# Kernel optimization log

Hardware: AMD Instinct MI355X
Metric: run time of the kernel (lower is better)

Reference implementation:

```python
import jax, jax.numpy as jnp
import numpy as np

B, BOARD, D = 2048, 19, 64
N = BOARD * BOARD
DIRS = ((-1, 0), (1, 0), (0, -1), (0, 1))


def _shift(x, dr, dc, fill):
    # shift a [B,H,W] grid by (dr,dc), filling off-board with `fill`
    p = jnp.pad(x, ((0, 0), (1, 1), (1, 1)), constant_values=fill)
    H, W = x.shape[1], x.shape[2]
    return p[:, 1 + dr:1 + dr + H, 1 + dc:1 + dc + W]


def _group_labels(color):
    # batched parallel connected components (min-label propagation + pointer jumping)
    # color: [B,H,W] int32, -1 = empty, 0 = black, 1 = white
    b, H, W = color.shape
    n = H * W
    init = jnp.broadcast_to(jnp.arange(n, dtype=jnp.int32).reshape(1, H, W), (b, H, W))

    def body(state):
        labels, _ = state
        m = labels
        for dr, dc in DIRS:
            nl = _shift(labels, dr, dc, n)          # neighbor label (n = sentinel)
            nc = _shift(color, dr, dc, -2)          # neighbor color (-2 = off-board)
            m = jnp.minimum(m, jnp.where(nc == color, nl, n))
        flat = m.reshape(b, n)
        # pointer jumping: label <- label[label]
        flat = jnp.minimum(flat, jnp.take_along_axis(flat, flat, axis=1))
        new = flat.reshape(b, H, W)
        return new, jnp.any(new != labels)

    labels, _ = jax.lax.while_loop(lambda s: s[1], body, (init, jnp.array(True)))
    return labels.reshape(b, n)


def setup_inputs() -> dict:
    key = jax.random.key(0)
    k1, k2, k3, k4 = jax.random.split(key, 4)
    col = jax.random.randint(k1, (B, BOARD, BOARD), 0, 3)  # 0 empty, 1 black, 2 white
    stones = jnp.stack([col == 1, col == 2], axis=1)        # [B,2,H,W] bool
    ko_points = jax.random.randint(k2, (B, 2), -1, BOARD).astype(jnp.int32)
    current_player = jax.random.randint(k3, (B,), 0, 2).astype(jnp.int32)
    features = jax.random.normal(k4, (B, N, D), dtype=jnp.float32)
    return {"stones": stones, "ko_points": ko_points,
            "current_player": current_player, "features": features}


def reference(stones, ko_points, current_player, features):
    stones = stones.astype(bool)
    black = stones[:, 0]
    white = stones[:, 1] & ~stones[:, 0]
    color = jnp.where(black, 0, jnp.where(white, 1, -1)).astype(jnp.int32)  # [B,H,W]
    b, H, W = color.shape
    n = H * W
    bidx = jnp.arange(b)

    labels = _group_labels(color)                 # [B,N] flat root index per point
    empty = color < 0
    stone = ~empty
    lab_grid = labels.reshape(b, H, W)

    # liberties per group root: each empty point contributes 1 per DISTINCT adjacent group
    neigh = []
    for dr, dc in DIRS:
        nl = _shift(lab_grid, dr, dc, n)
        ns = _shift(stone.astype(jnp.int32), dr, dc, 0) > 0
        neigh.append(jnp.where(empty & ns, nl, n).reshape(b, n))
    libs = jnp.zeros((b, n), dtype=jnp.int32)
    for i in range(4):
        li = neigh[i]
        dup = jnp.zeros(li.shape, dtype=bool)
        for j in range(i):
            dup = dup | (li == neigh[j])
        contrib = ((li < n) & ~dup).astype(jnp.int32)
        libs = libs.at[bidx[:, None], jnp.where(li < n, li, 0)].add(contrib)

    # legal moves = empty points minus ko point
    legal = empty.reshape(b, n)
    kr, kc = ko_points[:, 0].astype(jnp.int32), ko_points[:, 1].astype(jnp.int32)
    has_ko = kr >= 0
    ko_flat = jnp.clip(kr, 0, H - 1) * W + jnp.clip(kc, 0, W - 1)
    cur = legal[bidx, ko_flat]
    legal = legal.at[bidx, ko_flat].set(jnp.where(has_ko, False, cur))

    scores = jnp.stack([black.sum(axis=(1, 2)), white.sum(axis=(1, 2))], axis=1).astype(jnp.int32)

    # group sum-pooling of per-point features over union-find groups
    mask = stone.reshape(b, n).astype(features.dtype)[..., None]   # [B,N,1]
    pooled = jnp.zeros_like(features).at[bidx[:, None], labels].add(features * mask)
    out_feats = jnp.take_along_axis(pooled, labels[..., None], axis=1) * mask

    return out_feats, libs, legal, scores
```

## Files before the change

kernel.cpp:

```cpp
#include <hip/hip_runtime.h>


constexpr int BOARD = 19;
constexpr int NN = BOARD * BOARD;
constexpr int DD = 64;
constexpr int NT = 256;
constexpr int NW = NT / 64;
constexpr int NQ = NN * (DD / 4);

typedef float f4v __attribute__((ext_vector_type(4)));

__global__ __launch_bounds__(NT) void go_board(
    const int* __restrict__ stones,
    const int* __restrict__ ko,
    const float* __restrict__ feat,
    float* __restrict__ o_feats,
    float* __restrict__ o_libs,
    float* __restrict__ o_legal,
    float* __restrict__ o_scores)
{
    const int b = blockIdx.x;
    const int tid = threadIdx.x;

    __shared__ int s_color[NN];
    __shared__ int s_label[NN];
    __shared__ int s_libs[NN];
    __shared__ int s_cnt[NN];
    __shared__ int s_start[NN];
    __shared__ int s_ptr[NN];
    __shared__ int s_members[NN];
    __shared__ int s_glist[NN];
    __shared__ int s_gs[NN];
    __shared__ int s_gc[NN];
    __shared__ int s_ng;
    __shared__ int s_sc[2];
    __shared__ int s_changed;
    __shared__ unsigned int s_orw;

    if (tid == 0) { s_orw = 0u; s_sc[0] = 0; s_sc[1] = 0; s_ng = 0; }
    __syncthreads();

    {
        unsigned int acc = 0u;
        const unsigned int* w = (const unsigned int*)stones;
        for (int i = tid; i < 768; i += NT) acc |= w[i];
        for (int off = 32; off > 0; off >>= 1)
            acc |= (unsigned int)__shfl_xor((int)acc, off, 64);
        if ((tid & 63) == 0 && acc) atomicOr(&s_orw, acc);
    }
    __syncthreads();
    const unsigned int orw = s_orw;
    const int mode = (orw <= 1u) ? 0 : (((orw & 0xFEFEFEFEu) == 0u) ? 1 : 2);

    for (int i = tid; i < NN; i += NT) {
        int blk, wht;
        const size_t base = (size_t)b * (2 * NN);
        if (mode == 0) {
            blk = stones[base + i] != 0;
            wht = stones[base + NN + i] != 0;
        } else if (mode == 1) {
            const unsigned char* s8 = (const unsigned char*)stones;
            blk = s8[base + i] != 0;
            wht = s8[base + NN + i] != 0;
        } else {
            const float* sf = (const float*)stones;
            blk = sf[base + i] != 0.0f;
            wht = sf[base + NN + i] != 0.0f;
        }
        if (blk) wht = 0;
        s_color[i] = blk ? 0 : (wht ? 1 : -1);
        s_label[i] = i;
        s_libs[i] = 0;
        s_cnt[i] = 0;
    }

    for (int it = 0; it < 64; ++it) {
        __syncthreads();
        if (tid == 0) s_changed = 0;
        __syncthreads();
        for (int i = tid; i < NN; i += NT) {
            const int c = s_color[i];
            if (c >= 0) {
                int m = s_label[i];
                const int r = i / BOARD;
                const int q = i - r * BOARD;
                if (r > 0         && s_color[i - BOARD] == c) m = min(m, s_label[i - BOARD]);
                if (r < BOARD - 1 && s_color[i + BOARD] == c) m = min(m, s_label[i + BOARD]);
                if (q > 0         && s_color[i - 1] == c)     m = min(m, s_label[i - 1]);
                if (q < BOARD - 1 && s_color[i + 1] == c)     m = min(m, s_label[i + 1]);
                m = min(m, s_label[m]);
                if (m < s_label[i]) { s_label[i] = m; s_changed = 1; }
            }
        }
        __syncthreads();
        if (!s_changed) break;
    }

    for (int i = tid; i < NN; i += NT) {
        const int c = s_color[i];
        if (c < 0) {
            const int r = i / BOARD;
            const int q = i - r * BOARD;
            const int l0 = (r > 0         && s_color[i - BOARD] >= 0) ? s_label[i - BOARD] : NN;
            const int l1 = (r < BOARD - 1 && s_color[i + BOARD] >= 0) ? s_label[i + BOARD] : NN;
            const int l2 = (q > 0         && s_color[i - 1] >= 0)     ? s_label[i - 1]     : NN;
            const int l3 = (q < BOARD - 1 && s_color[i + 1] >= 0)     ? s_label[i + 1]     : NN;
            if (l0 < NN)                                     atomicAdd(&s_libs[l0], 1);
            if (l1 < NN && l1 != l0)                         atomicAdd(&s_libs[l1], 1);
            if (l2 < NN && l2 != l0 && l2 != l1)             atomicAdd(&s_libs[l2], 1);
            if (l3 < NN && l3 != l0 && l3 != l1 && l3 != l2) atomicAdd(&s_libs[l3], 1);
        } else {
            atomicAdd(&s_sc[c], 1);
            atomicAdd(&s_cnt[s_label[i]], 1);
            if (s_label[i] == i) {
                const int gi = atomicAdd(&s_ng, 1);
                s_glist[gi] = i;
            }
        }
    }
    __syncthreads();

    if (tid < 64) {
        int carry = 0;
        for (int c = 0; c < 6; ++c) {
            const int i = c * 64 + tid;
            const int v = (i < NN) ? s_cnt[i] : 0;
            int x = v;
            for (int off = 1; off < 64; off <<= 1) {
                const int y = __shfl_up(x, off, 64);
                if (tid >= off) x += y;
            }
            if (i < NN) { s_start[i] = carry + x - v; s_ptr[i] = carry + x - v; }
            carry += __shfl(x, 63, 64);
        }
    }
    __syncthreads();

    const int ng = s_ng;
    const int kr = ko[2 * b];
    const int kc = ko[2 * b + 1];
    for (int i = tid; i < NN; i += NT) {
        if (s_color[i] >= 0) {
            const int pos = atomicAdd(&s_ptr[s_label[i]], 1);
            s_members[pos] = i;
        }
        if (i < ng) {
            const int root = s_glist[i];
            s_gs[i] = s_start[root];
            s_gc[i] = s_cnt[root];
        }
        o_libs[(size_t)b * NN + i] = (float)s_libs[i];
        bool legal = (s_color[i] < 0);
        if (kr >= 0) {
            const int krr = min(max(kr, 0), BOARD - 1);
            const int kcc = min(max(kc, 0), BOARD - 1);
            if (i == krr * BOARD + kcc) legal = false;
        }
        o_legal[(size_t)b * NN + i] = legal ? 1.0f : 0.0f;
    }
    if (tid == 0) {
        o_scores[(size_t)b * 2 + 0] = (float)s_sc[0];
        o_scores[(size_t)b * 2 + 1] = (float)s_sc[1];
    }
    __syncthreads();

    const float4* f4 = (const float4*)feat + (size_t)b * NQ;
    f4v* o4 = (f4v*)o_feats + (size_t)b * NQ;
    const int wave = tid >> 6;
    const int lane = tid & 63;
    const int mi = lane >> 4;
    const int q  = lane & 15;
    for (int g = wave; g < ng; g += NW) {
        const int s = s_gs[g];
        const int cnt = s_gc[g];
        float4 acc = make_float4(0.f, 0.f, 0.f, 0.f);
        for (int k = mi; k < cnt; k += 4) {
            const float4 v = f4[s_members[s + k] * 16 + q];
            acc.x += v.x; acc.y += v.y; acc.z += v.z; acc.w += v.w;
        }
        acc.x += __shfl_xor(acc.x, 16); acc.y += __shfl_xor(acc.y, 16);
        acc.z += __shfl_xor(acc.z, 16); acc.w += __shfl_xor(acc.w, 16);
        acc.x += __shfl_xor(acc.x, 32); acc.y += __shfl_xor(acc.y, 32);
        acc.z += __shfl_xor(acc.z, 32); acc.w += __shfl_xor(acc.w, 32);
        const f4v av = {acc.x, acc.y, acc.z, acc.w};
        for (int k = mi; k < cnt; k += 4) {
            __builtin_nontemporal_store(av, &o4[s_members[s + k] * 16 + q]);
        }
    }
    const f4v z = {0.f, 0.f, 0.f, 0.f};
    for (int p = tid; p < NQ; p += NT) {
        const int cell = p >> 4;
        if (s_color[cell] < 0)
            __builtin_nontemporal_store(z, &o4[p]);
    }
}

extern "C" void kernel_launch(void* const* d_in, const int* in_sizes, int n_in,
                              void* d_out, int out_size, void* d_ws, size_t ws_size,
                              hipStream_t stream) {
    const int* stones = (const int*)d_in[0];
    const int* ko     = (const int*)d_in[1];
    const float* feat = (const float*)d_in[3];
    float* out        = (float*)d_out;

    const int B = in_sizes[2];

    float* o_feats  = out;
    float* o_libs   = o_feats + (size_t)B * NN * DD;
    float* o_legal  = o_libs  + (size_t)B * NN;
    float* o_scores = o_legal + (size_t)B * NN;

    go_board<<<B, NT, 0, stream>>>(stones, ko, feat,
                                   o_feats, o_libs, o_legal, o_scores);
}
```

Measured before the change: 68.37 us.

## Pack color and label into one LDS word, double sweep, early zero stores

Merges the separate color and label shared arrays into one packed word (color in the high bits, label in the low 10 bits), so each neighbour check needs one LDS read and one XOR compare. Each convergence iteration now runs two propagation sweeps, roughly halving the number of barrier-and-flag rounds. The zero-fill stores for empty cells are moved before the labeling loop so that global write traffic overlaps the LDS-bound union-find. Running two sweeps in place between barriers is a mild race that relies on min-label monotonicity to stay correct.

```diff
diff --git a/kernel.cpp b/kernel.cpp
--- a/kernel.cpp
+++ b/kernel.cpp
@@ -9,6 +9,7 @@
 constexpr int NQ = NN * (DD / 4);
 
 typedef float f4v __attribute__((ext_vector_type(4)));
+
 
 __global__ __launch_bounds__(NT) void go_board(
     const int* __restrict__ stones,
@@ -22,8 +23,7 @@
     const int b = blockIdx.x;
     const int tid = threadIdx.x;
 
-    __shared__ int s_color[NN];
-    __shared__ int s_label[NN];
+    __shared__ int s_cl[NN];
     __shared__ int s_libs[NN];
     __shared__ int s_cnt[NN];
     __shared__ int s_start[NN];
@@ -67,52 +67,68 @@
             blk = sf[base + i] != 0.0f;
             wht = sf[base + NN + i] != 0.0f;
         }
-        if (blk) wht = 0;
-        s_color[i] = blk ? 0 : (wht ? 1 : -1);
-        s_label[i] = i;
+        const int cc = blk ? 1 : ((wht && !blk) ? 2 : 0);
+        s_cl[i] = (cc << 10) | i;
         s_libs[i] = 0;
         s_cnt[i] = 0;
     }
-
+    __syncthreads();
+
+    f4v* o4 = (f4v*)o_feats + (size_t)b * NQ;
+    {
+        const f4v z = {0.f, 0.f, 0.f, 0.f};
+        for (int p = tid; p < NQ; p += NT) {
+            const int cell = p >> 4;
+            if ((s_cl[cell] >> 10) == 0)
+                __builtin_nontemporal_store(z, &o4[p]);
+        }
+    }
+
+    auto sweep = [&]() {
+        for (int i = tid; i < NN; i += NT) {
+            const int w = s_cl[i];
+            if (w >> 10) {
+                int m = w;
+                const int r = i / BOARD;
+                const int q = i - r * BOARD;
+                if (r > 0)         { const int nw = s_cl[i - BOARD]; if (!((nw ^ w) >> 10)) m = min(m, nw); }
+                if (r < BOARD - 1) { const int nw = s_cl[i + BOARD]; if (!((nw ^ w) >> 10)) m = min(m, nw); }
+                if (q > 0)         { const int nw = s_cl[i - 1];     if (!((nw ^ w) >> 10)) m = min(m, nw); }
+                if (q < BOARD - 1) { const int nw = s_cl[i + 1];     if (!((nw ^ w) >> 10)) m = min(m, nw); }
+                m = min(m, s_cl[m & 1023]);
+                if (m < w) { s_cl[i] = m; s_changed = 1; }
+            }
+        }
+    };
     for (int it = 0; it < 64; ++it) {
         __syncthreads();
         if (tid == 0) s_changed = 0;
         __syncthreads();
-        for (int i = tid; i < NN; i += NT) {
-            const int c = s_color[i];
-            if (c >= 0) {
-                int m = s_label[i];
-                const int r = i / BOARD;
-                const int q = i - r * BOARD;
-                if (r > 0         && s_color[i - BOARD] == c) m = min(m, s_label[i - BOARD]);
-                if (r < BOARD - 1 && s_color[i + BOARD] == c) m = min(m, s_label[i + BOARD]);
-                if (q > 0         && s_color[i - 1] == c)     m = min(m, s_label[i - 1]);
-                if (q < BOARD - 1 && s_color[i + 1] == c)     m = min(m, s_label[i + 1]);
-                m = min(m, s_label[m]);
-                if (m < s_label[i]) { s_label[i] = m; s_changed = 1; }
-            }
-        }
+        sweep();
+        sweep();
         __syncthreads();
         if (!s_changed) break;
     }
 
     for (int i = tid; i < NN; i += NT) {
-        const int c = s_color[i];
-        if (c < 0) {
+        const int w = s_cl[i];
+        if ((w >> 10) == 0) {
             const int r = i / BOARD;
             const int q = i - r * BOARD;
-            const int l0 = (r > 0         && s_color[i - BOARD] >= 0) ? s_label[i - BOARD] : NN;
-            const int l1 = (r < BOARD - 1 && s_color[i + BOARD] >= 0) ? s_label[i + BOARD] : NN;
-            const int l2 = (q > 0         && s_color[i - 1] >= 0)     ? s_label[i - 1]     : NN;
-            const int l3 = (q < BOARD - 1 && s_color[i + 1] >= 0)     ? s_label[i + 1]     : NN;
+            int l0 = NN, l1 = NN, l2 = NN, l3 = NN;
+            if (r > 0)         { const int nw = s_cl[i - BOARD]; if (nw >> 10) l0 = nw & 1023; }
+            if (r < BOARD - 1) { const int nw = s_cl[i + BOARD]; if (nw >> 10) l1 = nw & 1023; }
+            if (q > 0)         { const int nw = s_cl[i - 1];     if (nw >> 10) l2 = nw & 1023; }
+            if (q < BOARD - 1) { const int nw = s_cl[i + 1];     if (nw >> 10) l3 = nw & 1023; }
             if (l0 < NN)                                     atomicAdd(&s_libs[l0], 1);
             if (l1 < NN && l1 != l0)                         atomicAdd(&s_libs[l1], 1);
             if (l2 < NN && l2 != l0 && l2 != l1)             atomicAdd(&s_libs[l2], 1);
             if (l3 < NN && l3 != l0 && l3 != l1 && l3 != l2) atomicAdd(&s_libs[l3], 1);
         } else {
-            atomicAdd(&s_sc[c], 1);
-            atomicAdd(&s_cnt[s_label[i]], 1);
-            if (s_label[i] == i) {
+            atomicAdd(&s_sc[(w >> 10) - 1], 1);
+            const int lab = w & 1023;
+            atomicAdd(&s_cnt[lab], 1);
+            if (lab == i) {
                 const int gi = atomicAdd(&s_ng, 1);
                 s_glist[gi] = i;
             }
@@ -140,8 +156,9 @@
     const int kr = ko[2 * b];
     const int kc = ko[2 * b + 1];
     for (int i = tid; i < NN; i += NT) {
-        if (s_color[i] >= 0) {
-            const int pos = atomicAdd(&s_ptr[s_label[i]], 1);
+        const int w = s_cl[i];
+        if (w >> 10) {
+            const int pos = atomicAdd(&s_ptr[w & 1023], 1);
             s_members[pos] = i;
         }
         if (i < ng) {
@@ -150,7 +167,7 @@
             s_gc[i] = s_cnt[root];
         }
         o_libs[(size_t)b * NN + i] = (float)s_libs[i];
-        bool legal = (s_color[i] < 0);
+        bool legal = ((w >> 10) == 0);
         if (kr >= 0) {
             const int krr = min(max(kr, 0), BOARD - 1);
             const int kcc = min(max(kc, 0), BOARD - 1);
@@ -165,7 +182,6 @@
     __syncthreads();
 
     const float4* f4 = (const float4*)feat + (size_t)b * NQ;
-    f4v* o4 = (f4v*)o_feats + (size_t)b * NQ;
     const int wave = tid >> 6;
     const int lane = tid & 63;
     const int mi = lane >> 4;
@@ -187,12 +203,6 @@
             __builtin_nontemporal_store(av, &o4[s_members[s + k] * 16 + q]);
         }
     }
-    const f4v z = {0.f, 0.f, 0.f, 0.f};
-    for (int p = tid; p < NQ; p += NT) {
-        const int cell = p >> 4;
-        if (s_color[cell] < 0)
-            __builtin_nontemporal_store(z, &o4[p]);
-    }
 }
 
 extern "C" void kernel_launch(void* const* d_in, const int* in_sizes, int n_in,
```

New measurement: 64.60 us. -5.5%, faster.
